# Kernel optimization log

Hardware: AMD Instinct MI355X
Metric: run time of the kernel (lower is better)

The kernel has to match this reference:

```python
import jax, jax.numpy as jnp
import numpy as np

B, L, D, H, M = 2, 1024, 1024, 16, 64
DH = D // H  # depth per head


def setup_inputs() -> dict:
    key = jax.random.key(0)
    ks = jax.random.split(key, 7)
    s = 0.02
    return {
        "x": jax.random.normal(ks[0], (B, L, D), jnp.float32),
        "Wq": jax.random.normal(ks[1], (D, D), jnp.float32) * s,
        "Wk": jax.random.normal(ks[2], (D, D), jnp.float32) * s,
        "Wv": jax.random.normal(ks[3], (D, D), jnp.float32) * s,
        "Wo": jax.random.normal(ks[4], (D, D), jnp.float32) * s,
        "rel_k_table": jax.random.normal(ks[5], (2 * M + 1, DH), jnp.float32) * s,
        "rel_v_table": jax.random.normal(ks[6], (2 * M + 1, DH), jnp.float32) * s,
    }


def _rel_idx(length, max_rel):
    # Shaw-style clipped relative position indices: [L, L] in [0, 2*max_rel]
    r = jnp.arange(length)
    return jnp.clip(r[None, :] - r[:, None], -max_rel, max_rel) + max_rel


def _split_heads(t):
    # [B, L, D] -> [B, H, L, DH]
    return t.reshape(B, L, H, DH).transpose(0, 2, 1, 3)


def reference(x, Wq, Wk, Wv, Wo, rel_k_table, rel_v_table):
    q = _split_heads(x @ Wq) * (DH ** -0.5)  # T2T scales q by d_head^-0.5
    k = _split_heads(x @ Wk)
    v = _split_heads(x @ Wv)

    idx = _rel_idx(L, M)
    rel_k = rel_k_table[idx]  # [L, L, DH] gathered keys-relative embeddings
    rel_v = rel_v_table[idx]  # [L, L, DH]

    # _relative_attention_inner(q, k, rel_k, transpose=True)
    logits = jnp.einsum('bhid,bhjd->bhij', q, k) + jnp.einsum('bhid,ijd->bhij', q, rel_k)
    w = jax.nn.softmax(logits, axis=-1)  # [B, H, L, L]; dropout_rate=0 / inference

    # _relative_attention_inner(w, v, rel_v, transpose=False)
    o = jnp.einsum('bhij,bhjd->bhid', w, v) + jnp.einsum('bhij,ijd->bhid', w, rel_v)

    # combine heads then output transform
    o = o.transpose(0, 2, 1, 3).reshape(B, L, D)
    return o @ Wo
```

## Files before the change

### kernel.cpp

```cpp
#include <hip/hip_runtime.h>
#include <hip/hip_bf16.h>
#include <math.h>

#define B_ 2
#define L_ 1024
#define D_ 1024
#define H_ 16
#define DH_ 64
#define M_ 64
#define R_ 129
#define NLD ((size_t)B_ * L_ * D_)
#define DD  ((size_t)D_ * D_)
#define QSCALE 0.18033688011112042f

using bf16x8 = __attribute__((ext_vector_type(8))) short;
using f32x4  = __attribute__((ext_vector_type(4))) float;

__device__ __forceinline__ unsigned short f2bf(float f) {
    unsigned int x = __builtin_bit_cast(unsigned int, f);
    unsigned int r = x + 0x7fffu + ((x >> 16) & 1u);
    return (unsigned short)(r >> 16);
}
__device__ __forceinline__ float bf2f(unsigned short u) {
    unsigned int x = ((unsigned int)u) << 16;
    return __builtin_bit_cast(float, x);
}
__device__ __forceinline__ unsigned int pk2bf(float lo, float hi) {
    __hip_bfloat162 h = __float22bfloat162_rn(float2{lo, hi});
    unsigned int u;
    __builtin_memcpy(&u, &h, 4);
    return u;
}

__global__ __launch_bounds__(256)
void prep(const float* __restrict__ x,
          const float* __restrict__ W0, const float* __restrict__ W1,
          const float* __restrict__ W2, const float* __restrict__ W3,
          const float* __restrict__ relk, const float* __restrict__ relv,
          unsigned short* __restrict__ xb, unsigned short* __restrict__ Wt,
          unsigned short* __restrict__ relkb, unsigned short* __restrict__ relvT)
{
    __shared__ float tile[32][33];
    const int bid = blockIdx.x, t = threadIdx.x;
    if (bid < 2048) {
        const int i = bid * 256 + t;
        float4 v = ((const float4*)x)[i];
        short4 o = { (short)f2bf(v.x), (short)f2bf(v.y), (short)f2bf(v.z), (short)f2bf(v.w) };
        ((short4*)xb)[i] = o;
    } else if (bid < 6144) {
        const int wb = bid - 2048;
        const int z = wb >> 10, rem = wb & 1023;
        const float* W = z == 0 ? W0 : z == 1 ? W1 : z == 2 ? W2 : W3;
        unsigned short* T = Wt + (size_t)z * DD;
        const int k0 = (rem >> 5) * 32, n0 = (rem & 31) * 32;
        const int r = t >> 3, c = (t & 7) * 4;
        float4 v = *(const float4*)&W[(size_t)(k0 + r) * D_ + n0 + c];
        tile[r][c] = v.x; tile[r][c + 1] = v.y; tile[r][c + 2] = v.z; tile[r][c + 3] = v.w;
        __syncthreads();
        short4 o = { (short)f2bf(tile[c][r]),     (short)f2bf(tile[c + 1][r]),
                     (short)f2bf(tile[c + 2][r]), (short)f2bf(tile[c + 3][r]) };
        *(short4*)&T[(size_t)(n0 + r) * D_ + k0 + c] = o;
    } else {
        const int idx = (bid - 6144) * 256 + t;
        if (idx < 144 * 64) {
            const int r = idx >> 6, d = idx & 63;
            relkb[idx] = (r < R_) ? f2bf(relk[r * 64 + d]) : (unsigned short)0;
        }
        if (idx < 64 * 136) {
            const int d = idx / 136, r = idx - d * 136;
            relvT[idx] = (r < R_) ? f2bf(relv[r * 64 + d]) : (unsigned short)0;
        }
    }
}

__global__ __launch_bounds__(256)
void gemm64(const unsigned short* __restrict__ A, const unsigned short* __restrict__ Bt,
            unsigned short* __restrict__ Cb, float* __restrict__ Cf, float scale0)
{
    __shared__ unsigned short As[64][64];
    __shared__ unsigned short Bs[128][64];

    const int t = threadIdx.x, lane = t & 63, wid = t >> 6;
    const int fr = lane & 15, g = lane >> 4;
    const int m0 = blockIdx.y * 64;
    const int nglob = blockIdx.x * 128;
    const int mat = nglob >> 10;
    const int n0 = nglob & 1023;
    const float scale = (mat == 0) ? scale0 : 1.f;
    const int wm = (wid >> 1) * 32, wn = (wid & 1) * 64;

    f32x4 acc[2][4] = {};

    int arow[2], akof[2], adst[2];
#pragma unroll
    for (int c = 0; c < 2; ++c) {
        const int chunk = c * 256 + t;
        arow[c] = chunk >> 3;
        akof[c] = ((chunk & 7) ^ (arow[c] & 7)) * 8;
        adst[c] = chunk * 8;
    }
    int brow[4], bkof[4], bdst[4];
#pragma unroll
    for (int c = 0; c < 4; ++c) {
        const int chunk = c * 256 + t;
        brow[c] = chunk >> 3;
        bkof[c] = ((chunk & 7) ^ (brow[c] & 7)) * 8;
        bdst[c] = chunk * 8;
    }

    const unsigned short* Abase = A  + (size_t)m0 * D_;
    const unsigned short* Bbase = Bt + (size_t)nglob * D_;

    for (int k0 = 0; k0 < D_; k0 += 64) {
        __syncthreads();
#pragma unroll
        for (int c = 0; c < 2; ++c)
            __builtin_amdgcn_global_load_lds(
                (const __attribute__((address_space(1))) void*)(Abase + (size_t)arow[c] * D_ + k0 + akof[c]),
                (__attribute__((address_space(3))) void*)(&As[0][0] + adst[c]), 16, 0, 0);
#pragma unroll
        for (int c = 0; c < 4; ++c)
            __builtin_amdgcn_global_load_lds(
                (const __attribute__((address_space(1))) void*)(Bbase + (size_t)brow[c] * D_ + k0 + bkof[c]),
                (__attribute__((address_space(3))) void*)(&Bs[0][0] + bdst[c]), 16, 0, 0);
        __syncthreads();

#pragma unroll
        for (int kb = 0; kb < 2; ++kb) {
            bf16x8 av[2], bv[4];
#pragma unroll
            for (int i = 0; i < 2; ++i) {
                const int ra = wm + i * 16 + fr;
                av[i] = *(const bf16x8*)&As[ra][(((kb << 2) + g) ^ (ra & 7)) * 8];
            }
#pragma unroll
            for (int j = 0; j < 4; ++j) {
                const int rb = wn + j * 16 + fr;
                bv[j] = *(const bf16x8*)&Bs[rb][(((kb << 2) + g) ^ (rb & 7)) * 8];
            }
#pragma unroll
            for (int i = 0; i < 2; ++i)
#pragma unroll
                for (int j = 0; j < 4; ++j)
                    acc[i][j] = __builtin_amdgcn_mfma_f32_16x16x32_bf16(av[i], bv[j], acc[i][j], 0, 0, 0);
        }
    }

    const int orow = g * 4;
    if (Cb) {
        unsigned short* Cp = Cb + (size_t)mat * NLD;
#pragma unroll
        for (int i = 0; i < 2; ++i)
#pragma unroll
            for (int j = 0; j < 4; ++j) {
                unsigned short* cp = Cp + (size_t)(m0 + wm + i * 16 + orow) * D_ + n0 + wn + j * 16 + fr;
#pragma unroll
                for (int rg = 0; rg < 4; ++rg)
                    cp[(size_t)rg * D_] = f2bf(acc[i][j][rg] * scale);
            }
    } else {
#pragma unroll
        for (int i = 0; i < 2; ++i)
#pragma unroll
            for (int j = 0; j < 4; ++j) {
                float* cp = Cf + (size_t)(m0 + wm + i * 16 + orow) * D_ + n0 + wn + j * 16 + fr;
#pragma unroll
                for (int rg = 0; rg < 4; ++rg)
                    cp[(size_t)rg * D_] = acc[i][j][rg] * scale;
            }
    }
}

__device__ __forceinline__ void stage_k(const unsigned short* src, unsigned short* dst, int t)
{
#pragma unroll
    for (int it = 0; it < 2; ++it) {
        const int c = it * 256 + t;
        const int j = c >> 3;
        const int sc = (c & 7) ^ (j & 7);
        __builtin_amdgcn_global_load_lds(
            (const __attribute__((address_space(1))) void*)(src + (size_t)j * D_ + sc * 8),
            (__attribute__((address_space(3))) void*)(dst + c * 8), 16, 0, 0);
    }
}

__device__ __forceinline__ void write_vt(unsigned short (*Vtl)[64], int jp, int d0, bf16x8 a, bf16x8 b)
{
    const int jlo = (2 * jp) & 7;
    const int jc  = jp >> 2;
#pragma unroll
    for (int e = 0; e < 8; ++e) {
        const int d = d0 + e;
        const unsigned int val = (unsigned int)(unsigned short)a[e]
                               | ((unsigned int)(unsigned short)b[e] << 16);
        *(unsigned int*)&Vtl[d][((jc ^ (d & 7)) << 3) + jlo] = val;
    }
}

__global__ __launch_bounds__(256)
void attn_mfma(const unsigned short* __restrict__ Qb, const unsigned short* __restrict__ Kb,
               const unsigned short* __restrict__ Vb,
               const unsigned short* __restrict__ relkb,
               const unsigned short* __restrict__ relvT,
               const float* __restrict__ relv,
               unsigned short* __restrict__ Ob)
{
    __shared__ unsigned short Klds[2][64][64];
    __shared__ unsigned short Vt[2][64][64];
    __shared__ unsigned short Plds[64][72];
    __shared__ unsigned short QRs[64][136];
    __shared__ unsigned short Wsum[64][136];

    const int t    = threadIdx.x;
    const int lane = t & 63;
    const int w    = t >> 6;
    const int fr   = lane & 15;
    const int g    = lane >> 4;

    const int bx  = blockIdx.x;
    const int xcd = bx & 7, slot = bx >> 3;
    const int bh  = (xcd << 2) | (slot >> 4);
    const int rb  = slot & 15;
    const int b   = bh >> 4, h = bh & 15;
    const int i0  = rb * 64;
    const size_t head = (size_t)b * L_ * D_ + (size_t)h * DH_;

    const int iloc = w * 16 + fr;

    const unsigned short* Kh = Kb + head;
    const unsigned short* Vh = Vb + head;

    stage_k(Kh, &Klds[0][0][0], t);

    const int jp = t & 31, d0v = ((t >> 5) & 7) * 8;
    bf16x8 va  = *(const bf16x8*)(Vh + (size_t)(2 * jp) * D_ + d0v);
    bf16x8 vb2 = *(const bf16x8*)(Vh + (size_t)(2 * jp + 1) * D_ + d0v);

    {
        unsigned int* wp = (unsigned int*)&Wsum[0][0];
        for (int i = t; i < 64 * 136 / 2; i += 256) wp[i] = 0u;
    }

    bf16x8 qf[2];
    {
        const unsigned short* qp = Qb + head + (size_t)(i0 + iloc) * D_;
        qf[0] = *(const bf16x8*)(qp + g * 8);
        qf[1] = *(const bf16x8*)(qp + 32 + g * 8);
    }

#pragma unroll
    for (int rc = 0; rc < 9; ++rc) {
        f32x4 acc = {};
#pragma unroll
        for (int kb = 0; kb < 2; ++kb) {
            bf16x8 rv = *(const bf16x8*)&relkb[(size_t)(rc * 16 + fr) * 64 + kb * 32 + g * 8];
            acc = __builtin_amdgcn_mfma_f32_16x16x32_bf16(rv, qf[kb], acc, 0, 0, 0);
        }
        if (rc < 8) {
            uint2 pk = { pk2bf(acc[0], acc[1]), pk2bf(acc[2], acc[3]) };
            *(uint2*)&QRs[iloc][rc * 16 + g * 4] = pk;
        } else if (g == 0) {
            QRs[iloc][128] = f2bf(acc[0]);
        }
    }

    write_vt(Vt[0], jp, d0v, va, vb2);
    asm volatile("s_waitcnt vmcnt(0)" ::: "memory");
    __syncthreads();

    const float qr0   = bf2f(QRs[iloc][0]);
    const float qr128 = bf2f(QRs[iloc][128]);

    f32x4 oacc[4] = {};
    float lpart = 0.f, pe0p = 0.f, pe128p = 0.f;

    int bb = 0;
    for (int jt = 0; jt < 16; ++jt) {
        const bool pre = (jt < 15);
        if (pre) {
            stage_k(Kh + (size_t)(jt + 1) * 64 * D_, &Klds[bb ^ 1][0][0], t);
            const unsigned short* vp = Vh + (size_t)((jt + 1) * 64 + 2 * jp) * D_ + d0v;
            va  = *(const bf16x8*)vp;
            vb2 = *(const bf16x8*)(vp + D_);
        }

        f32x4 s[4];
        __builtin_amdgcn_s_setprio(1);
#pragma unroll
        for (int fc = 0; fc < 4; ++fc) {
            f32x4 a = {};
            const int j = fc * 16 + fr;
#pragma unroll
            for (int kb = 0; kb < 2; ++kb) {
                bf16x8 kv = *(const bf16x8*)&Klds[bb][j][(((kb << 2) + g) ^ (j & 7)) * 8];
                a = __builtin_amdgcn_mfma_f32_16x16x32_bf16(kv, qf[kb], a, 0, 0, 0);
            }
            s[fc] = a;
        }
        __builtin_amdgcn_s_setprio(0);

        bf16x8 vv0[4], vv1[4];
#pragma unroll
        for (int fd = 0; fd < 4; ++fd) {
            const int d = fd * 16 + fr;
            vv0[fd] = *(const bf16x8*)&Vt[bb][d][((g)     ^ (d & 7)) * 8];
            vv1[fd] = *(const bf16x8*)&Vt[bb][d][((4 + g) ^ (d & 7)) * 8];
        }

        const int dt   = (jt - rb) * 64;
        const int relb = dt - iloc + g * 4;

        if (dt <= -128 || dt >= 128) {
            const float qrc = (dt < 0) ? qr0 : qr128;
            float tsum = 0.f;
#pragma unroll
            for (int fc = 0; fc < 4; ++fc) {
                float p0 = exp2f(s[fc][0] + qrc);
                float p1 = exp2f(s[fc][1] + qrc);
                float p2 = exp2f(s[fc][2] + qrc);
                float p3 = exp2f(s[fc][3] + qrc);
                uint2 pk = { pk2bf(p0, p1), pk2bf(p2, p3) };
                *(uint2*)&Plds[iloc][fc * 16 + g * 4] = pk;
                tsum += (p0 + p1) + (p2 + p3);
            }
            lpart += tsum;
            if (dt < 0) pe0p += tsum; else pe128p += tsum;
        } else if (dt == 0) {
#pragma unroll
            for (int fc = 0; fc < 4; ++fc) {
                const int c0 = relb + fc * 16 + M_;
                float pe[4];
#pragma unroll
                for (int reg = 0; reg < 4; ++reg) {
                    pe[reg] = exp2f(s[fc][reg] + bf2f(QRs[iloc][c0 + reg]));
                    lpart += pe[reg];
                }
                uint2 pk = { pk2bf(pe[0], pe[1]), pk2bf(pe[2], pe[3]) };
                *(uint2*)&Plds[iloc][fc * 16 + g * 4] = pk;
                Wsum[iloc][c0 + 0] = (unsigned short)(pk.x & 0xffffu);
                Wsum[iloc][c0 + 1] = (unsigned short)(pk.x >> 16);
                Wsum[iloc][c0 + 2] = (unsigned short)(pk.y & 0xffffu);
                Wsum[iloc][c0 + 3] = (unsigned short)(pk.y >> 16);
            }
        } else {
#pragma unroll
            for (int fc = 0; fc < 4; ++fc) {
                float pe[4];
#pragma unroll
                for (int reg = 0; reg < 4; ++reg) {
                    const int colr = relb + fc * 16 + reg + M_;
                    const int col  = colr < 0 ? 0 : (colr > 128 ? 128 : colr);
                    pe[reg] = exp2f(s[fc][reg] + bf2f(QRs[iloc][col]));
                    lpart += pe[reg];
                    if (col == 0)        pe0p   += pe[reg];
                    else if (col == 128) pe128p += pe[reg];
                    else                 Wsum[iloc][col] = f2bf(pe[reg]);
                }
                uint2 pk = { pk2bf(pe[0], pe[1]), pk2bf(pe[2], pe[3]) };
                *(uint2*)&Plds[iloc][fc * 16 + g * 4] = pk;
            }
        }

        asm volatile("s_waitcnt lgkmcnt(0)" ::: "memory");
        __builtin_amdgcn_sched_barrier(0);

        bf16x8 pa0 = *(const bf16x8*)&Plds[iloc][g * 8];
        bf16x8 pa1 = *(const bf16x8*)&Plds[iloc][32 + g * 8];
        __builtin_amdgcn_s_setprio(1);
#pragma unroll
        for (int fd = 0; fd < 4; ++fd) {
            oacc[fd] = __builtin_amdgcn_mfma_f32_16x16x32_bf16(pa0, vv0[fd], oacc[fd], 0, 0, 0);
            oacc[fd] = __builtin_amdgcn_mfma_f32_16x16x32_bf16(pa1, vv1[fd], oacc[fd], 0, 0, 0);
        }
        __builtin_amdgcn_s_setprio(0);

        if (pre) write_vt(Vt[bb ^ 1], jp, d0v, va, vb2);
        asm volatile("s_waitcnt vmcnt(0)" ::: "memory");
        __syncthreads();
        bb ^= 1;
    }

    lpart  += __shfl_xor(lpart, 16);  lpart  += __shfl_xor(lpart, 32);
    pe0p   += __shfl_xor(pe0p, 16);   pe0p   += __shfl_xor(pe0p, 32);
    pe128p += __shfl_xor(pe128p, 16); pe128p += __shfl_xor(pe128p, 32);
    if (g == 0) {
        Wsum[iloc][0]   = f2bf(pe0p);
        Wsum[iloc][128] = f2bf(pe128p);
    }
    asm volatile("s_waitcnt lgkmcnt(0)" ::: "memory");
    __builtin_amdgcn_sched_barrier(0);

#pragma unroll
    for (int kc = 0; kc < 4; ++kc) {
        bf16x8 wa = *(const bf16x8*)&Wsum[iloc][kc * 32 + g * 8];
#pragma unroll
        for (int fd = 0; fd < 4; ++fd) {
            bf16x8 rv = *(const bf16x8*)&relvT[(size_t)(fd * 16 + fr) * 136 + kc * 32 + g * 8];
            oacc[fd] = __builtin_amdgcn_mfma_f32_16x16x32_bf16(wa, rv, oacc[fd], 0, 0, 0);
        }
    }

    float invd[4], pr128[4];
#pragma unroll
    for (int reg = 0; reg < 4; ++reg) {
        const int src = (lane & 48) | (g * 4 + reg);
        invd[reg]  = 1.f / __shfl(lpart, src, 64);
        pr128[reg] = __shfl(pe128p, src, 64);
    }

#pragma unroll
    for (int fd = 0; fd < 4; ++fd) {
        const float r128 = relv[128 * 64 + fd * 16 + fr];
        unsigned short* op = Ob + head + (size_t)(i0 + w * 16 + g * 4) * D_ + fd * 16 + fr;
#pragma unroll
        for (int reg = 0; reg < 4; ++reg)
            op[(size_t)reg * D_] = f2bf((oacc[fd][reg] + pr128[reg] * r128) * invd[reg]);
    }
}

extern "C" void kernel_launch(void* const* d_in, const int* in_sizes, int n_in,
                              void* d_out, int out_size, void* d_ws, size_t ws_size,
                              hipStream_t stream)
{
    const float* x    = (const float*)d_in[0];
    const float* Wq   = (const float*)d_in[1];
    const float* Wk   = (const float*)d_in[2];
    const float* Wv   = (const float*)d_in[3];
    const float* Wo   = (const float*)d_in[4];
    const float* relk = (const float*)d_in[5];
    const float* relv = (const float*)d_in[6];
    float* out = (float*)d_out;

    unsigned short* xb    = (unsigned short*)d_ws;
    unsigned short* Wt    = xb + NLD;
    unsigned short* relkb = Wt + 4 * DD;
    unsigned short* relvT = relkb + 144 * 64;
    unsigned short* QKVb  = relvT + 64 * 136;
    unsigned short* Ob    = QKVb + 3 * NLD;

    prep<<<dim3(6180), 256, 0, stream>>>(x, Wq, Wk, Wv, Wo, relk, relv, xb, Wt, relkb, relvT);

    gemm64<<<dim3(24, 32), 256, 0, stream>>>(xb, Wt, QKVb, nullptr, QSCALE);

    attn_mfma<<<dim3(512), 256, 0, stream>>>(QKVb, QKVb + NLD, QKVb + 2 * NLD,
                                             relkb, relvT, relv, Ob);

    gemm64<<<dim3(8, 32), 256, 0, stream>>>(Ob, Wt + 3 * DD, nullptr, out, 1.f);
}
```

Measured before the change: 82.44 us.

## Alias QR and weight-sum LDS buffers and single-buffer V tile to cut LDS

Merges the relative-logit buffer QRs and the weight accumulator Wsum into one shared array, overwriting each column in place once it has been read, and zeroes only the columns that no key position ever reaches for the first and last row blocks. The V transpose tile is single-buffered, with an extra barrier before the next tile is written. Together these shrink LDS per block, presumably to fit more blocks per CU, at the cost of one more barrier per key tile. Correctness relies on each column being read before it is overwritten within a row.

```diff
diff --git a/kernel.cpp b/kernel.cpp
--- a/kernel.cpp
+++ b/kernel.cpp
@@ -206,10 +206,9 @@
                unsigned short* __restrict__ Ob)
 {
     __shared__ unsigned short Klds[2][64][64];
-    __shared__ unsigned short Vt[2][64][64];
+    __shared__ unsigned short Vt[64][64];
     __shared__ unsigned short Plds[64][72];
-    __shared__ unsigned short QRs[64][136];
-    __shared__ unsigned short Wsum[64][136];
+    __shared__ unsigned short QW[64][136];
 
     const int t    = threadIdx.x;
     const int lane = t & 63;
@@ -236,11 +235,6 @@
     bf16x8 va  = *(const bf16x8*)(Vh + (size_t)(2 * jp) * D_ + d0v);
     bf16x8 vb2 = *(const bf16x8*)(Vh + (size_t)(2 * jp + 1) * D_ + d0v);
 
-    {
-        unsigned int* wp = (unsigned int*)&Wsum[0][0];
-        for (int i = t; i < 64 * 136 / 2; i += 256) wp[i] = 0u;
-    }
-
     bf16x8 qf[2];
     {
         const unsigned short* qp = Qb + head + (size_t)(i0 + iloc) * D_;
@@ -258,18 +252,23 @@
         }
         if (rc < 8) {
             uint2 pk = { pk2bf(acc[0], acc[1]), pk2bf(acc[2], acc[3]) };
-            *(uint2*)&QRs[iloc][rc * 16 + g * 4] = pk;
+            *(uint2*)&QW[iloc][rc * 16 + g * 4] = pk;
         } else if (g == 0) {
-            QRs[iloc][128] = f2bf(acc[0]);
-        }
-    }
-
-    write_vt(Vt[0], jp, d0v, va, vb2);
+            QW[iloc][128] = f2bf(acc[0]);
+        }
+    }
+    if (rb == 0) {
+        for (int c = 1 + g; c <= 63 - iloc; c += 4) QW[iloc][c] = 0;
+    } else if (rb == 15) {
+        for (int c = 128 - iloc + g; c <= 127; c += 4) QW[iloc][c] = 0;
+    }
+
+    write_vt(Vt, jp, d0v, va, vb2);
     asm volatile("s_waitcnt vmcnt(0)" ::: "memory");
     __syncthreads();
 
-    const float qr0   = bf2f(QRs[iloc][0]);
-    const float qr128 = bf2f(QRs[iloc][128]);
+    const float qr0   = bf2f(QW[iloc][0]);
+    const float qr128 = bf2f(QW[iloc][128]);
 
     f32x4 oacc[4] = {};
     float lpart = 0.f, pe0p = 0.f, pe128p = 0.f;
@@ -303,8 +302,8 @@
 #pragma unroll
         for (int fd = 0; fd < 4; ++fd) {
             const int d = fd * 16 + fr;
-            vv0[fd] = *(const bf16x8*)&Vt[bb][d][((g)     ^ (d & 7)) * 8];
-            vv1[fd] = *(const bf16x8*)&Vt[bb][d][((4 + g) ^ (d & 7)) * 8];
+            vv0[fd] = *(const bf16x8*)&Vt[d][((g)     ^ (d & 7)) * 8];
+            vv1[fd] = *(const bf16x8*)&Vt[d][((4 + g) ^ (d & 7)) * 8];
         }
 
         const int dt   = (jt - rb) * 64;
@@ -332,15 +331,15 @@
                 float pe[4];
 #pragma unroll
                 for (int reg = 0; reg < 4; ++reg) {
-                    pe[reg] = exp2f(s[fc][reg] + bf2f(QRs[iloc][c0 + reg]));
+                    pe[reg] = exp2f(s[fc][reg] + bf2f(QW[iloc][c0 + reg]));
                     lpart += pe[reg];
                 }
                 uint2 pk = { pk2bf(pe[0], pe[1]), pk2bf(pe[2], pe[3]) };
                 *(uint2*)&Plds[iloc][fc * 16 + g * 4] = pk;
-                Wsum[iloc][c0 + 0] = (unsigned short)(pk.x & 0xffffu);
-                Wsum[iloc][c0 + 1] = (unsigned short)(pk.x >> 16);
-                Wsum[iloc][c0 + 2] = (unsigned short)(pk.y & 0xffffu);
-                Wsum[iloc][c0 + 3] = (unsigned short)(pk.y >> 16);
+                QW[iloc][c0 + 0] = (unsigned short)(pk.x & 0xffffu);
+                QW[iloc][c0 + 1] = (unsigned short)(pk.x >> 16);
+                QW[iloc][c0 + 2] = (unsigned short)(pk.y & 0xffffu);
+                QW[iloc][c0 + 3] = (unsigned short)(pk.y >> 16);
             }
         } else {
 #pragma unroll
@@ -350,11 +349,11 @@
                 for (int reg = 0; reg < 4; ++reg) {
                     const int colr = relb + fc * 16 + reg + M_;
                     const int col  = colr < 0 ? 0 : (colr > 128 ? 128 : colr);
-                    pe[reg] = exp2f(s[fc][reg] + bf2f(QRs[iloc][col]));
+                    pe[reg] = exp2f(s[fc][reg] + bf2f(QW[iloc][col]));
                     lpart += pe[reg];
                     if (col == 0)        pe0p   += pe[reg];
                     else if (col == 128) pe128p += pe[reg];
-                    else                 Wsum[iloc][col] = f2bf(pe[reg]);
+                    else                 QW[iloc][col] = f2bf(pe[reg]);
                 }
                 uint2 pk = { pk2bf(pe[0], pe[1]), pk2bf(pe[2], pe[3]) };
                 *(uint2*)&Plds[iloc][fc * 16 + g * 4] = pk;
@@ -374,7 +373,11 @@
         }
         __builtin_amdgcn_s_setprio(0);
 
-        if (pre) write_vt(Vt[bb ^ 1], jp, d0v, va, vb2);
+        if (pre) {
+            asm volatile("s_waitcnt lgkmcnt(0)" ::: "memory");
+            __builtin_amdgcn_s_barrier();
+            write_vt(Vt, jp, d0v, va, vb2);
+        }
         asm volatile("s_waitcnt vmcnt(0)" ::: "memory");
         __syncthreads();
         bb ^= 1;
@@ -384,15 +387,15 @@
     pe0p   += __shfl_xor(pe0p, 16);   pe0p   += __shfl_xor(pe0p, 32);
     pe128p += __shfl_xor(pe128p, 16); pe128p += __shfl_xor(pe128p, 32);
     if (g == 0) {
-        Wsum[iloc][0]   = f2bf(pe0p);
-        Wsum[iloc][128] = f2bf(pe128p);
+        QW[iloc][0]   = f2bf(pe0p);
+        QW[iloc][128] = f2bf(pe128p);
     }
     asm volatile("s_waitcnt lgkmcnt(0)" ::: "memory");
     __builtin_amdgcn_sched_barrier(0);
 
 #pragma unroll
     for (int kc = 0; kc < 4; ++kc) {
-        bf16x8 wa = *(const bf16x8*)&Wsum[iloc][kc * 32 + g * 8];
+        bf16x8 wa = *(const bf16x8*)&QW[iloc][kc * 32 + g * 8];
 #pragma unroll
         for (int fd = 0; fd < 4; ++fd) {
             bf16x8 rv = *(const bf16x8*)&relvT[(size_t)(fd * 16 + fr) * 136 + kc * 32 + g * 8];
```

After: 81.70 us. Within noise of the previous version (-0.9%).
